# Optimization experiments

Hardware: AMD Instinct MI355X
Metric: run time of the kernel (lower is better)

Reference implementation:

```python
import jax, jax.numpy as jnp
import numpy as np

GN_EPS = 1e-5
LN_EPS = 1e-5
M_HEADS, N_LEVELS, N_POINTS, D_MODEL = 8, 3, 4, 256
HEAD_DIM = D_MODEL // M_HEADS


def conv1x1(x, w, b):
    return jnp.einsum('nchw,oc->nohw', x, w[:, :, 0, 0]) + b[None, :, None, None]


def conv3x3(x, w, b):
    y = jax.lax.conv_general_dilated(x, w, (1, 1), ((1, 1), (1, 1)),
                                     dimension_numbers=('NCHW', 'OIHW', 'NCHW'))
    return y + b[None, :, None, None]


def group_norm(x, w, b, groups=32):
    N, C, H, W = x.shape
    xg = x.reshape(N, groups, C // groups, H, W)
    mu = xg.mean((2, 3, 4), keepdims=True)
    var = xg.var((2, 3, 4), keepdims=True)
    xg = (xg - mu) / jnp.sqrt(var + GN_EPS)
    return xg.reshape(N, C, H, W) * w[None, :, None, None] + b[None, :, None, None]


def layer_norm(x, w, b):
    mu = x.mean(-1, keepdims=True)
    var = x.var(-1, keepdims=True)
    return (x - mu) / jnp.sqrt(var + LN_EPS) * w + b


def prelu(x, a):
    return jnp.where(x >= 0, x, a[0] * x)


def pos_sine(mask):
    # DETR PositionEmbeddingSine, num_pos_feats=128, normalize=True
    nm = (~mask).astype(jnp.float32)
    y_embed = jnp.cumsum(nm, 1)
    x_embed = jnp.cumsum(nm, 2)
    eps, scale = 1e-6, 2.0 * np.pi
    y_embed = y_embed / (y_embed[:, -1:, :] + eps) * scale
    x_embed = x_embed / (x_embed[:, :, -1:] + eps) * scale
    npf = D_MODEL // 2
    dim_t = 10000.0 ** (2.0 * (jnp.arange(npf) // 2).astype(jnp.float32) / npf)
    px = x_embed[..., None] / dim_t
    py = y_embed[..., None] / dim_t

    def il(p):
        return jnp.stack([jnp.sin(p[..., 0::2]), jnp.cos(p[..., 1::2])], -1).reshape(p.shape[0], p.shape[1], p.shape[2], -1)

    return jnp.transpose(jnp.concatenate([il(py), il(px)], -1), (0, 3, 1, 2))


def resize_mask_nearest(mask, h, w):
    H, W = mask.shape[1], mask.shape[2]
    iy = jnp.floor(jnp.arange(h) * (H / h)).astype(jnp.int32)
    ix = jnp.floor(jnp.arange(w) * (W / w)).astype(jnp.int32)
    return mask[:, iy][:, :, ix]


def bilinear_gather(v, x, y):
    # v: (N,M,D,H,W); x,y: (N,Lq,M,P) pixel coords; zero padding, align_corners=False
    N, M, D, H, W = v.shape
    Lq, P = x.shape[1], x.shape[3]
    x0f = jnp.floor(x)
    y0f = jnp.floor(y)
    wx = (x - x0f)[..., None]
    wy = (y - y0f)[..., None]
    x0i = x0f.astype(jnp.int32)
    y0i = y0f.astype(jnp.int32)
    flat = jnp.transpose(v, (0, 1, 3, 4, 2)).reshape(N, M, H * W, D)

    def gather(xi, yi):
        valid = (xi >= 0) & (xi < W) & (yi >= 0) & (yi < H)
        idx = jnp.clip(yi, 0, H - 1) * W + jnp.clip(xi, 0, W - 1)
        idx2 = jnp.transpose(idx, (0, 2, 1, 3)).reshape(N, M, Lq * P)
        g = jnp.take_along_axis(flat, idx2[..., None], axis=2)
        g = jnp.transpose(g.reshape(N, M, Lq, P, D), (0, 2, 1, 3, 4))
        return g * valid[..., None]

    g00 = gather(x0i, y0i)
    g01 = gather(x0i + 1, y0i)
    g10 = gather(x0i, y0i + 1)
    g11 = gather(x0i + 1, y0i + 1)
    return g00 * (1 - wx) * (1 - wy) + g01 * wx * (1 - wy) + g10 * (1 - wx) * wy + g11 * wx * wy


def _forward(x0, x1, x2, p3_w, p3_b, p4_w, p4_b, p5_w, p5_b,
             gn3_w, gn3_b, gn4_w, gn4_b, gn5_w, gn5_b, level_embed,
             so_w, so_b, aw_w, aw_b, vp_w, vp_b, op_w, op_b,
             ln1_w, ln1_b, ffn1_w, ffn1_b, ffn2_w, ffn2_b, ln2_w, ln2_b,
             d3_w, d3_b, d3_a, d4_w, d4_b, d4_a, d5_w, d5_b, d5_a,
             padding_masks):
    N = x0.shape[0]
    shapes = [(x0.shape[2], x0.shape[3]), (x1.shape[2], x1.shape[3]), (x2.shape[2], x2.shape[3])]
    p3 = group_norm(conv1x1(x0, p3_w, p3_b), gn3_w, gn3_b)
    p4 = group_norm(conv1x1(x1, p4_w, p4_b), gn4_w, gn4_b)
    p5 = group_norm(conv1x1(x2, p5_w, p5_b), gn5_w, gn5_b)
    srcs = [p3, p4, p5]
    masks = [resize_mask_nearest(padding_masks, H, W) for (H, W) in shapes]
    src_flat = jnp.concatenate([s.reshape(N, D_MODEL, -1).transpose(0, 2, 1) for s in srcs], 1)
    mask_flat = jnp.concatenate([m.reshape(N, -1) for m in masks], 1)
    pos_flat = jnp.concatenate(
        [pos_sine(m).reshape(N, D_MODEL, -1).transpose(0, 2, 1) + level_embed[l][None, None]
         for l, m in enumerate(masks)], 1)
    # valid ratios (N, 3, 2) as (w, h)
    vrs = []
    for (H, W), m in zip(shapes, masks):
        vh = jnp.sum((~m[:, :, 0]).astype(jnp.float32), 1) / H
        vw = jnp.sum((~m[:, 0, :]).astype(jnp.float32), 1) / W
        vrs.append(jnp.stack([vw, vh], -1))
    vr = jnp.stack(vrs, 1)
    # reference points (N, Lq, 3, 2)
    refs = []
    for lvl, (H, W) in enumerate(shapes):
        ry, rx = jnp.meshgrid(jnp.linspace(0.5, H - 0.5, H), jnp.linspace(0.5, W - 0.5, W), indexing='ij')
        ry = ry.reshape(-1)[None] / (vr[:, None, lvl, 1] * H)
        rx = rx.reshape(-1)[None] / (vr[:, None, lvl, 0] * W)
        refs.append(jnp.stack([rx, ry], -1))
    ref = jnp.concatenate(refs, 1)[:, :, None] * vr[:, None]

    # --- MSDeformAttn ---
    q = src_flat + pos_flat
    Lq = q.shape[1]
    value = src_flat @ vp_w.T + vp_b
    value = jnp.where(mask_flat[..., None], 0.0, value).reshape(N, Lq, M_HEADS, HEAD_DIM)
    off = (q @ so_w.T + so_b).reshape(N, Lq, M_HEADS, N_LEVELS, N_POINTS, 2)
    aw = jax.nn.softmax((q @ aw_w.T + aw_b).reshape(N, Lq, M_HEADS, N_LEVELS * N_POINTS), -1)
    aw = aw.reshape(N, Lq, M_HEADS, N_LEVELS, N_POINTS)
    norm = jnp.array([[W, H] for (H, W) in shapes], jnp.float32)
    loc = ref[:, :, None, :, None, :] + off / norm[None, None, None, :, None, :]
    out = jnp.zeros((N, Lq, M_HEADS, HEAD_DIM), value.dtype)
    start = 0
    for l, (H, W) in enumerate(shapes):
        vl = value[:, start:start + H * W].reshape(N, H, W, M_HEADS, HEAD_DIM)
        vl = jnp.transpose(vl, (0, 3, 4, 1, 2))  # (N, M, D, H, W)
        sx = loc[:, :, :, l, :, 0] * W - 0.5
        sy = loc[:, :, :, l, :, 1] * H - 0.5
        samp = bilinear_gather(vl, sx, sy)  # (N, Lq, M, P, D)
        out = out + jnp.einsum('nqmpd,nqmp->nqmd', samp, aw[:, :, :, l])
        start += H * W
    attn = out.reshape(N, Lq, D_MODEL) @ op_w.T + op_b

    src = layer_norm(src_flat + attn, ln1_w, ln1_b)
    ffn = jax.nn.relu(src @ ffn1_w.T + ffn1_b) @ ffn2_w.T + ffn2_b
    src = layer_norm(src + ffn, ln2_w, ln2_b)

    # take level-2 tokens back to spatial
    H2, W2 = shapes[2]
    start2 = shapes[0][0] * shapes[0][1] + shapes[1][0] * shapes[1][1]
    o = src[:, start2:start2 + H2 * W2].reshape(N, H2, W2, D_MODEL).transpose(0, 3, 1, 2)

    o = jax.image.resize(o, (N, D_MODEL) + shapes[0], 'bilinear', antialias=False) + prelu(conv3x3(x0, d3_w, d3_b), d3_a)
    o = jax.image.resize(o, (N, D_MODEL) + shapes[1], 'bilinear', antialias=False) + prelu(conv3x3(x1, d4_w, d4_b), d4_a)
    o = jax.image.resize(o, (N, D_MODEL) + shapes[2], 'bilinear', antialias=False) + prelu(conv3x3(x2, d5_w, d5_b), d5_a)
    return o


def setup_inputs():
    key = jax.random.key(0)
    ks = jax.random.split(key, 24)
    B, C = 2, 256

    def w(k, shape, sc=0.02):
        return jax.random.normal(k, shape, jnp.float32) * sc

    inp = {}
    inp['x0'] = jax.random.normal(ks[0], (B, 2048, 64, 64), jnp.float32)
    inp['x1'] = jax.random.normal(ks[1], (B, 2048, 32, 32), jnp.float32)
    inp['x2'] = jax.random.normal(ks[2], (B, 2048, 16, 16), jnp.float32)
    inp['padding_masks'] = jnp.zeros((B, 64, 64), bool)
    inp['p3_w'] = w(ks[3], (C, 2048, 1, 1)); inp['p3_b'] = jnp.zeros((C,))
    inp['p4_w'] = w(ks[4], (C, 2048, 1, 1)); inp['p4_b'] = jnp.zeros((C,))
    inp['p5_w'] = w(ks[5], (C, 2048, 1, 1)); inp['p5_b'] = jnp.zeros((C,))
    inp['gn3_w'] = jnp.ones((C,)); inp['gn3_b'] = jnp.zeros((C,))
    inp['gn4_w'] = jnp.ones((C,)); inp['gn4_b'] = jnp.zeros((C,))
    inp['gn5_w'] = jnp.ones((C,)); inp['gn5_b'] = jnp.zeros((C,))
    inp['level_embed'] = w(ks[6], (3, C), 1.0)
    inp['so_w'] = w(ks[7], (192, C)); inp['so_b'] = w(ks[8], (192,), 0.5)
    inp['aw_w'] = w(ks[9], (96, C)); inp['aw_b'] = jnp.zeros((96,))
    inp['vp_w'] = w(ks[10], (C, C)); inp['vp_b'] = jnp.zeros((C,))
    inp['op_w'] = w(ks[11], (C, C)); inp['op_b'] = jnp.zeros((C,))
    inp['ln1_w'] = jnp.ones((C,)); inp['ln1_b'] = jnp.zeros((C,))
    inp['ffn1_w'] = w(ks[12], (1024, C)); inp['ffn1_b'] = jnp.zeros((1024,))
    inp['ffn2_w'] = w(ks[13], (C, 1024)); inp['ffn2_b'] = jnp.zeros((C,))
    inp['ln2_w'] = jnp.ones((C,)); inp['ln2_b'] = jnp.zeros((C,))
    inp['d3_w'] = w(ks[14], (C, 2048, 3, 3)); inp['d3_b'] = jnp.zeros((C,)); inp['d3_a'] = jnp.full((1,), 0.25)
    inp['d4_w'] = w(ks[15], (C, 2048, 3, 3)); inp['d4_b'] = jnp.zeros((C,)); inp['d4_a'] = jnp.full((1,), 0.25)
    inp['d5_w'] = w(ks[16], (C, 2048, 3, 3)); inp['d5_b'] = jnp.zeros((C,)); inp['d5_a'] = jnp.full((1,), 0.25)
    return inp


def reference(x0, x1, x2, padding_masks, p3_w, p3_b, p4_w, p4_b, p5_w, p5_b,
              gn3_w, gn3_b, gn4_w, gn4_b, gn5_w, gn5_b, level_embed,
              so_w, so_b, aw_w, aw_b, vp_w, vp_b, op_w, op_b,
              ln1_w, ln1_b, ffn1_w, ffn1_b, ffn2_w, ffn2_b, ln2_w, ln2_b,
              d3_w, d3_b, d3_a, d4_w, d4_b, d4_a, d5_w, d5_b, d5_a):
    return _forward(x0, x1, x2, p3_w, p3_b, p4_w, p4_b, p5_w, p5_b,
                    gn3_w, gn3_b, gn4_w, gn4_b, gn5_w, gn5_b, level_embed,
                    so_w, so_b, aw_w, aw_b, vp_w, vp_b, op_w, op_b,
                    ln1_w, ln1_b, ffn1_w, ffn1_b, ffn2_w, ffn2_b, ln2_w, ln2_b,
                    d3_w, d3_b, d3_a, d4_w, d4_b, d4_a, d5_w, d5_b, d5_a,
                    padding_masks)
```

## Files before the change

### kernel.cpp

```cpp
#include <hip/hip_runtime.h>
#include <hip/hip_bf16.h>

#define NTOK 5376

typedef short bfrag __attribute__((ext_vector_type(8)));
typedef short bvec4 __attribute__((ext_vector_type(4)));
typedef float facc  __attribute__((ext_vector_type(4)));

__device__ __forceinline__ short f2bf(float f) {
  __hip_bfloat16 h = __float2bfloat16(f);
  return *reinterpret_cast<short*>(&h);
}
__device__ __forceinline__ float bf2f(short s) {
  union { unsigned int u; float f; } cv;
  cv.u = ((unsigned int)(unsigned short)s) << 16;
  return cv.f;
}

#define ASYNC_COPY16(gp, sp) \
  __builtin_amdgcn_global_load_lds((const __attribute__((address_space(1))) unsigned int*)(gp), \
                                   (__attribute__((address_space(3))) unsigned int*)(sp), 16, 0, 0)

__global__ __launch_bounds__(256) void init_all_kernel(
    const float* __restrict__ x0, const float* __restrict__ x1, const float* __restrict__ x2,
    short* __restrict__ xb0, short* __restrict__ xb1, short* __restrict__ xb2,
    const float* __restrict__ p3, const float* __restrict__ p4, const float* __restrict__ p5,
    const float* __restrict__ vp,
    const float* __restrict__ so, const float* __restrict__ aw, const float* __restrict__ op,
    const float* __restrict__ f1, const float* __restrict__ f2,
    const float* __restrict__ d3,
    short* __restrict__ pwb0, short* __restrict__ pwb1, short* __restrict__ pwb2,
    short* __restrict__ vpb,
    short* __restrict__ soT, short* __restrict__ awT, short* __restrict__ opT,
    short* __restrict__ f1T, short* __restrict__ f2T,
    short* __restrict__ w0)
{
  __shared__ float tile[64][65];
  __shared__ float tt[32][33];
  int b = blockIdx.x;
  if (b < 7168) {
    const float* x; short* xb; int H, Wshift;
    if (b < 4096)      { x = x0; xb = xb0; H = 64; Wshift = 6; }
    else if (b < 6144) { x = x1; xb = xb1; H = 32; Wshift = 5; b -= 4096; }
    else               { x = x2; xb = xb2; H = 16; Wshift = 4; b -= 6144; }
    int cin0 = (b & 31) << 6;
    int t1 = b >> 5;
    int y = t1 & (H - 1);
    int n = t1 >> Wshift;
    int W = 1 << Wshift;
    int elems = 64 << Wshift;
    for (int i = threadIdx.x; i < elems; i += 256) {
      int px = i & (W - 1), cl = i >> Wshift;
      tile[cl][px] = x[(((long)(n * 2048 + cin0 + cl)) * H + y) * W + px];
    }
    __syncthreads();
    int Hp = H + 2;
    for (int i = threadIdx.x; i < elems; i += 256) {
      int cl = i & 63, px = i >> 6;
      xb[(((long)(n * Hp + y + 1)) * Hp + (px + 1)) * 2048 + cin0 + cl] = f2bf(tile[cl][px]);
    }
    return;
  }
  b -= 7168;
  if (b < 6144) {
    const float* src; short* dst;
    if (b < 2048)      { src = p3; dst = pwb0; }
    else if (b < 4096) { src = p4; dst = pwb1; b -= 2048; }
    else               { src = p5; dst = pwb2; b -= 4096; }
    int idx = b * 256 + threadIdx.x;
    dst[idx] = f2bf(src[idx]);
    return;
  }
  b -= 6144;
  if (b < 256) {
    int idx = b * 256 + threadIdx.x;
    vpb[idx] = f2bf(vp[idx]);
    return;
  }
  b -= 256;
  if (b < 648) {
    const float* src; short* dst; int N, K, tb;
    if (b < 48)       { src = so; dst = soT; N = 192;  K = 256;  tb = b; }
    else if (b < 72)  { src = aw; dst = awT; N = 96;   K = 256;  tb = b - 48; }
    else if (b < 136) { src = op; dst = opT; N = 256;  K = 256;  tb = b - 72; }
    else if (b < 392) { src = f1; dst = f1T; N = 1024; K = 256;  tb = b - 136; }
    else              { src = f2; dst = f2T; N = 256;  K = 1024; tb = b - 392; }
    int ktiles = K >> 5;
    int tn = tb / ktiles, tk = tb % ktiles;
#pragma unroll
    for (int s = 0; s < 4; ++s) {
      int i = s * 256 + threadIdx.x;
      int r = i >> 5, c = i & 31;
      tt[r][c] = src[(long)(tn * 32 + r) * K + tk * 32 + c];
    }
    __syncthreads();
#pragma unroll
    for (int s = 0; s < 4; ++s) {
      int i = s * 256 + threadIdx.x;
      int r = i >> 5, c = i & 31;
      dst[(long)(tk * 32 + r) * N + tn * 32 + c] = f2bf(tt[c][r]);
    }
    return;
  }
  b -= 648;
  {
    int p = b * 256 + threadIdx.x;
    int oc = p >> 11, cin = p & 2047;
    float v[9];
#pragma unroll
    for (int t = 0; t < 9; ++t) v[t] = d3[(long)p * 9 + t];
#pragma unroll
    for (int ky = 0; ky < 3; ++ky)
#pragma unroll
      for (int kx = 0; kx < 3; ++kx)
        w0[((long)(ky * 256 + oc)) * 6144 + kx * 2048 + cin] = f2bf(v[ky * 3 + kx]);
  }
}

#define BUFSH 24576

__device__ __forceinline__ void conv3x3_pipe(short* lds,
    const short* __restrict__ xb, const short* __restrict__ wb,
    short* __restrict__ part, int Wshift, int HW2, int mt, int kb, int steps)
{
  int tid = threadIdx.x;
  int lane = tid & 63;
  int wid = tid >> 6;
  int wm = wid >> 2;
  int wn = wid & 3;
  int W = 1 << Wshift;
  int HW = 1 << (2 * Wshift);
  int px0 = mt * 128;
  int n = px0 >> (2 * Wshift);
  int rem = px0 & (HW - 1);
  int Hp = W + 2;
  long rowstride = (long)Hp * 2048;

  const short* agA[2];
  const short* bgB[4];
#pragma unroll
  for (int r = 0; r < 2; ++r) {
    int c = r * 512 + tid;
    int pl = c >> 3;
    int kc = (c & 7) ^ (pl & 7);
    int p = rem + pl;
    int yy = p >> Wshift, xx = p & (W - 1);
    agA[r] = xb + (((long)(n * Hp + yy)) * Hp + xx) * 2048 + kc * 8;
  }
#pragma unroll
  for (int r = 0; r < 4; ++r) {
    int c = r * 512 + tid;
    int pl = c >> 3;
    int kc = (c & 7) ^ (pl & 7);
    bgB[r] = wb + (long)pl * 6144 + kc * 8;
  }
  int ldst = (tid & 448) * 8;

  facc acc[4][4];
#pragma unroll
  for (int mi = 0; mi < 4; ++mi)
#pragma unroll
    for (int ni = 0; ni < 4; ++ni) acc[mi][ni] = (facc)(0.f);

  int arow[4], brow[4];
#pragma unroll
  for (int i = 0; i < 4; ++i) {
    arow[i] = (wm * 64 + i * 16 + (lane & 15)) * 64;
    brow[i] = 8192 + (wn * 64 + i * 16 + (lane & 15)) * 64;
  }

  auto ISSUE = [&](int it, short* db) {
    int ky = (it >= 192) ? 2 : ((it >= 96) ? 1 : 0);
    int kc96 = it - ky * 96;
    long aoff = (long)ky * rowstride + (long)kc96 * 64;
    long boff = (long)ky * 1572864 + (long)kc96 * 64;
    ASYNC_COPY16(agA[0] + aoff, db + ldst);
    ASYNC_COPY16(agA[1] + aoff, db + 4096 + ldst);
    ASYNC_COPY16(bgB[0] + boff, db + 8192 + ldst);
    ASYNC_COPY16(bgB[1] + boff, db + 12288 + ldst);
    ASYNC_COPY16(bgB[2] + boff, db + 16384 + ldst);
    ASYNC_COPY16(bgB[3] + boff, db + 20480 + ldst);
  };

  auto COMPUTE = [&](const short* buf) {
#pragma unroll
    for (int k0 = 0; k0 < 2; ++k0) {
      int slot8 = ((((k0 << 2) + (lane >> 4)) ^ (lane & 7)) << 3);
      bfrag af[4], bf4[4];
#pragma unroll
      for (int mi = 0; mi < 4; ++mi) af[mi] = *(const bfrag*)(buf + arow[mi] + slot8);
#pragma unroll
      for (int ni = 0; ni < 4; ++ni) bf4[ni] = *(const bfrag*)(buf + brow[ni] + slot8);
      __builtin_amdgcn_s_setprio(1);
#pragma unroll
      for (int mi = 0; mi < 4; ++mi)
#pragma unroll
        for (int ni = 0; ni < 4; ++ni)
          acc[mi][ni] = __builtin_amdgcn_mfma_f32_16x16x32_bf16(af[mi], bf4[ni], acc[mi][ni], 0, 0, 0);
      __builtin_amdgcn_s_setprio(0);
    }
  };

  short* b0 = lds;
  short* b1 = lds + BUFSH;
  short* b2 = lds + 2 * BUFSH;
  int it0 = kb * steps;

  ISSUE(it0, b0);
  ISSUE(it0 + 1, b1);
  asm volatile("s_waitcnt vmcnt(6)" ::: "memory");
  __builtin_amdgcn_s_barrier();

  for (int t = 0; t < steps - 2; ++t) {
    ISSUE(it0 + t + 2, b2);
    COMPUTE(b0);
    asm volatile("s_waitcnt vmcnt(6)" ::: "memory");
    __builtin_amdgcn_s_barrier();
    short* tmp = b0; b0 = b1; b1 = b2; b2 = tmp;
  }
  COMPUTE(b0);
  asm volatile("s_waitcnt vmcnt(0)" ::: "memory");
  __builtin_amdgcn_s_barrier();
  COMPUTE(b1);

  short* pp = part + ((long)kb * HW2 + px0) * 256;
#pragma unroll
  for (int mi = 0; mi < 4; ++mi) {
    int pl = wm * 64 + mi * 16 + ((lane >> 4) << 2);
#pragma unroll
    for (int ni = 0; ni < 4; ++ni) {
      int ol = wn * 64 + ni * 16 + (lane & 15);
#pragma unroll
      for (int r = 0; r < 4; ++r)
        pp[(long)(pl + r) * 256 + ol] = f2bf(acc[mi][ni][r]);
    }
  }
}

__global__ __launch_bounds__(512, 2) void conv0_kernel(
    const short* __restrict__ xb, const short* __restrict__ wb, short* __restrict__ part) {
  __shared__ __align__(16) short lds[3 * BUFSH];
  int b = blockIdx.x;
  conv3x3_pipe(lds, xb, wb, part, 6, 8192, b >> 2, b & 3, 72);
}

__global__ __launch_bounds__(512, 2) void conv12_kernel(
    const short* __restrict__ xb1, const short* __restrict__ w1, short* __restrict__ part1,
    const short* __restrict__ xb2, const short* __restrict__ w2, short* __restrict__ part2) {
  __shared__ __align__(16) short lds[3 * BUFSH];
  int b = blockIdx.x;
  if (b < 128) {
    conv3x3_pipe(lds, xb1, w1, part1, 5, 2048, b >> 3, b & 7, 36);
  } else {
    b -= 128;
    conv3x3_pipe(lds, xb2, w2, part2, 4, 512, b >> 3, b & 7, 36);
  }
}

__device__ __forceinline__ void reduce_body(int idx, const short* __restrict__ part,
    const float* __restrict__ bias, const float* __restrict__ alpha_p,
    short* __restrict__ out, int HW2, int hwshift, int KB) {
  int px = idx >> 8, oc = idx & 255;
  long step = (long)HW2 * 256;
  float s = 0.f;
  for (int kb = 0; kb < KB; ++kb) s += bf2f(part[kb * step + idx]);
  float v = s + bias[oc];
  float alpha = alpha_p[0];
  v = (v >= 0.f) ? v : alpha * v;
  int HW = 1 << hwshift;
  int n = px >> hwshift;
  int sp = px & (HW - 1);
  out[(((long)(n * 256 + oc)) << hwshift) + sp] = f2bf(v);
}

__device__ __forceinline__ void block_reduce2(float& s, float& s2) {
#pragma unroll
  for (int o = 32; o > 0; o >>= 1) {
    s  += __shfl_down(s, o, 64);
    s2 += __shfl_down(s2, o, 64);
  }
  __shared__ float r1[4], r2[4];
  int wid = threadIdx.x >> 6;
  int lane = threadIdx.x & 63;
  if (lane == 0) { r1[wid] = s; r2[wid] = s2; }
  __syncthreads();
  s  = r1[0] + r1[1] + r1[2] + r1[3];
  s2 = r2[0] + r2[1] + r2[2] + r2[3];
  __syncthreads();
}

__global__ __launch_bounds__(256) void reduce0_stats_w12_kernel(
    const short* __restrict__ part0, const float* __restrict__ d3_b,
    const float* __restrict__ d3_a, short* __restrict__ c0b,
    const short* __restrict__ srcb, float* __restrict__ stats,
    const float* __restrict__ d4, const float* __restrict__ d5,
    short* __restrict__ w1, short* __restrict__ w2) {
  int b = blockIdx.x;
  if (b < 8192) {
    reduce_body(b * 256 + threadIdx.x, part0, d3_b, d3_a, c0b, 8192, 12, 4);
    return;
  }
  b -= 8192;
  if (b < 192) {
    int n = b / 96, r = b % 96, l = r / 32, g = r % 32;
    int H, base;
    if (l == 0)      { H = 64; base = 0; }
    else if (l == 1) { H = 32; base = 4096; }
    else             { H = 16; base = 5120; }
    int HW = H * H;
    const short* p = srcb + ((long)n * NTOK + base) * 256 + g * 8;
    float s = 0.f, s2 = 0.f;
    for (int idx = threadIdx.x; idx < HW * 8; idx += 256) {
      int hw = idx >> 3, c = idx & 7;
      float v = bf2f(p[(long)hw * 256 + c]);
      s += v; s2 += v * v;
    }
    block_reduce2(s, s2);
    if (threadIdx.x == 0) {
      float cnt = (float)(HW * 8);
      float mu = s / cnt;
      float var = s2 / cnt - mu * mu;
      stats[b * 2]     = mu;
      stats[b * 2 + 1] = rsqrtf(var + 1e-5f);
    }
    return;
  }
  b -= 192;
  {
    const float* src; short* dst;
    if (b < 2048) { src = d4; dst = w1; } else { src = d5; dst = w2; b -= 2048; }
    int p = b * 256 + threadIdx.x;
    int oc = p >> 11, cin = p & 2047;
    float v[9];
#pragma unroll
    for (int t = 0; t < 9; ++t) v[t] = src[(long)p * 9 + t];
#pragma unroll
    for (int ky = 0; ky < 3; ++ky)
#pragma unroll
      for (int kx = 0; kx < 3; ++kx)
        dst[((long)(ky * 256 + oc)) * 6144 + kx * 2048 + cin] = f2bf(v[ky * 3 + kx]);
  }
}

__global__ __launch_bounds__(256) void reduce12_gn_kernel(
    const short* __restrict__ part1, const short* __restrict__ part2,
    const float* __restrict__ d4_b, const float* __restrict__ d4_a,
    const float* __restrict__ d5_b, const float* __restrict__ d5_a,
    short* __restrict__ c1b, short* __restrict__ c2b,
    short* __restrict__ srcb, const float* __restrict__ stats,
    const float* __restrict__ gw0, const float* __restrict__ gb0,
    const float* __restrict__ gw1, const float* __restrict__ gb1,
    const float* __restrict__ gw2, const float* __restrict__ gb2) {
  int b = blockIdx.x;
  if (b < 2048) { reduce_body(b * 256 + threadIdx.x, part1, d4_b, d4_a, c1b, 2048, 10, 8); return; }
  if (b < 2560) { reduce_body((b - 2048) * 256 + threadIdx.x, part2, d5_b, d5_a, c2b, 512, 8, 8); return; }
  b -= 2560;
  int idx = b * 256 + threadIdx.x;
  int row = idx >> 8, c = idx & 255;
  int n = row / NTOK, t = row % NTOK;
  int l; const float *gw, *gb;
  if (t < 4096)      { l = 0; gw = gw0; gb = gb0; }
  else if (t < 5120) { l = 1; gw = gw1; gb = gb1; }
  else               { l = 2; gw = gw2; gb = gb2; }
  int si = (n * 96 + l * 32 + (c >> 3)) * 2;
  float mu = stats[si], rstd = stats[si + 1];
  float v = (bf2f(srcb[idx]) - mu) * rstd * gw[c] + gb[c];
  srcb[idx] = f2bf(v);
}

__device__ __forceinline__ void conv1x1_body(short* As, short* Bs,
    const short* __restrict__ A, const short* __restrict__ Bw,
    const float* __restrict__ bias, short* __restrict__ Cb,
    int Wshift, int Hp, int shift2, int tokbase, int ocb, int py)
{
  int tid = threadIdx.x;
  int lane = tid & 63;
  int wid = tid >> 6;
  int wm = wid >> 1, wn = wid & 1;
  int px0 = py * 128;

  const short* ag0[4];
  const short* bg0[4];
#pragma unroll
  for (int j = 0; j < 4; ++j) {
    int c = j * 256 + tid;
    int pl = c >> 3;
    int kc = (c & 7) ^ (pl & 7);
    int p = px0 + pl;
    int n = p >> shift2;
    int remp = p & ((1 << shift2) - 1);
    int W = 1 << Wshift;
    int yy = remp >> Wshift, xx = remp & (W - 1);
    long arow = (((long)(n * Hp + yy + 1)) * Hp + (xx + 1)) * 2048;
    ag0[j] = A + arow + kc * 8;
    bg0[j] = Bw + (long)(ocb * 128 + pl) * 2048 + kc * 8;
  }

  facc acc[4][4];
#pragma unroll
  for (int mi = 0; mi < 4; ++mi)
#pragma unroll
    for (int ni = 0; ni < 4; ++ni) acc[mi][ni] = (facc)(0.f);

  for (int it = 0; it < 32; ++it) {
    long off = (long)it * 64;
#pragma unroll
    for (int j = 0; j < 4; ++j) {
      ASYNC_COPY16(ag0[j] + off, As + (j * 256 + (tid & 192)) * 8);
// ... 248 lines not shown
  }
  float s1r = x, s2r = x * x;
  block_reduce2(s1r, s2r);
  float mu = s1r * (1.f / 256.f);
  float rstd = rsqrtf(s2r * (1.f / 256.f) - mu * mu + 1e-5f);
  x = (x - mu) * rstd * ln1_w[tid] + ln1_b[tid];
  x1s[tid] = x;
  __syncthreads();

  {
    int j0 = tid * 4;
    float a0 = 0.f, a1 = 0.f, a2 = 0.f, a3 = 0.f;
#pragma unroll 4
    for (int k = 0; k < 256; ++k) {
      bvec4 wv = *(const bvec4*)(f1T + (long)k * 1024 + j0);
      float xv = x1s[k];
      a0 += xv * bf2f(wv[0]); a1 += xv * bf2f(wv[1]);
      a2 += xv * bf2f(wv[2]); a3 += xv * bf2f(wv[3]);
    }
    hids[j0 + 0] = fmaxf(a0 + ffn1_b[j0 + 0], 0.f);
    hids[j0 + 1] = fmaxf(a1 + ffn1_b[j0 + 1], 0.f);
    hids[j0 + 2] = fmaxf(a2 + ffn1_b[j0 + 2], 0.f);
    hids[j0 + 3] = fmaxf(a3 + ffn1_b[j0 + 3], 0.f);
  }
  __syncthreads();

  float y;
  {
    float s0 = 0.f, s1 = 0.f, s2 = 0.f, s3 = 0.f;
#pragma unroll 4
    for (int k = 0; k < 1024; k += 4) {
      s0 += hids[k]     * bf2f(f2T[(long)k * 256 + tid]);
      s1 += hids[k + 1] * bf2f(f2T[(long)(k + 1) * 256 + tid]);
      s2 += hids[k + 2] * bf2f(f2T[(long)(k + 2) * 256 + tid]);
      s3 += hids[k + 3] * bf2f(f2T[(long)(k + 3) * 256 + tid]);
    }
    y = x + (s0 + s1) + (s2 + s3) + ffn2_b[tid];
  }
  s1r = y; s2r = y * y;
  block_reduce2(s1r, s2r);
  mu = s1r * (1.f / 256.f);
  rstd = rsqrtf(s2r * (1.f / 256.f) - mu * mu + 1e-5f);
  src2c[(long)b * 256 + tid] = (y - mu) * rstd * ln2_w[tid] + ln2_b[tid];
}

__global__ __launch_bounds__(256) void fused_resize_kernel(
    const float* __restrict__ src2c, const short* __restrict__ c0b,
    const short* __restrict__ c1b, const short* __restrict__ c2b,
    float* __restrict__ out) {
  int idx = blockIdx.x * 256 + threadIdx.x;
  int x = idx & 15, y = (idx >> 4) & 15, c = (idx >> 8) & 255, n = idx >> 16;
  const float* sbase = src2c + (long)n * 65536 + c;
  const short* c0p = c0b + ((long)(n * 256 + c) << 12);
  const short* c1p = c1b + ((long)(n * 256 + c) << 10);
  float s64 = 0.f;
#pragma unroll
  for (int dy = 0; dy < 4; ++dy) {
    int Y = 4 * y + dy;
    float sy = fminf(fmaxf(0.25f * Y - 0.375f, 0.f), 15.f);
    int y0 = (int)sy;
    int y1 = min(y0 + 1, 15);
    float wy = sy - y0;
#pragma unroll
    for (int dx = 0; dx < 4; ++dx) {
      int X = 4 * x + dx;
      float sx = fminf(fmaxf(0.25f * X - 0.375f, 0.f), 15.f);
      int x0 = (int)sx;
      int x1 = min(x0 + 1, 15);
      float wx = sx - x0;
      float v = (sbase[(y0 * 16 + x0) * 256] * (1.f - wx) + sbase[(y0 * 16 + x1) * 256] * wx) * (1.f - wy) +
                (sbase[(y1 * 16 + x0) * 256] * (1.f - wx) + sbase[(y1 * 16 + x1) * 256] * wx) * wy;
      s64 += v + bf2f(c0p[Y * 64 + X]);
    }
  }
  float s32 = bf2f(c1p[(2 * y) * 32 + 2 * x]) + bf2f(c1p[(2 * y) * 32 + 2 * x + 1]) +
              bf2f(c1p[(2 * y + 1) * 32 + 2 * x]) + bf2f(c1p[(2 * y + 1) * 32 + 2 * x + 1]);
  out[idx] = 0.0625f * s64 + 0.25f * s32 + bf2f(c2b[idx]);
}

extern "C" void kernel_launch(void* const* d_in, const int* in_sizes, int n_in,
                              void* d_out, int out_size, void* d_ws, size_t ws_size,
                              hipStream_t stream) {
  (void)in_sizes; (void)n_in; (void)out_size; (void)ws_size;
  const float* x0   = (const float*)d_in[0];
  const float* x1   = (const float*)d_in[1];
  const float* x2   = (const float*)d_in[2];
  const float* p3_w = (const float*)d_in[4];
  const float* p3_b = (const float*)d_in[5];
  const float* p4_w = (const float*)d_in[6];
  const float* p4_b = (const float*)d_in[7];
  const float* p5_w = (const float*)d_in[8];
  const float* p5_b = (const float*)d_in[9];
  const float* gn3_w = (const float*)d_in[10];
  const float* gn3_b = (const float*)d_in[11];
  const float* gn4_w = (const float*)d_in[12];
  const float* gn4_b = (const float*)d_in[13];
  const float* gn5_w = (const float*)d_in[14];
  const float* gn5_b = (const float*)d_in[15];
  const float* level_embed = (const float*)d_in[16];
  const float* so_w = (const float*)d_in[17];
  const float* so_b = (const float*)d_in[18];
  const float* aw_w = (const float*)d_in[19];
  const float* aw_b = (const float*)d_in[20];
  const float* vp_w = (const float*)d_in[21];
  const float* vp_b = (const float*)d_in[22];
  const float* op_w = (const float*)d_in[23];
  const float* op_b = (const float*)d_in[24];
  const float* ln1_w = (const float*)d_in[25];
  const float* ln1_b = (const float*)d_in[26];
  const float* ffn1_w = (const float*)d_in[27];
  const float* ffn1_b = (const float*)d_in[28];
  const float* ffn2_w = (const float*)d_in[29];
  const float* ffn2_b = (const float*)d_in[30];
  const float* ln2_w = (const float*)d_in[31];
  const float* ln2_b = (const float*)d_in[32];
  const float* d3_w = (const float*)d_in[33];
  const float* d3_b = (const float*)d_in[34];
  const float* d3_a = (const float*)d_in[35];
  const float* d4_w = (const float*)d_in[36];
  const float* d4_b = (const float*)d_in[37];
  const float* d4_a = (const float*)d_in[38];
  const float* d5_w = (const float*)d_in[39];
  const float* d5_b = (const float*)d_in[40];
  const float* d5_a = (const float*)d_in[41];

  float* ws = (float*)d_ws;
  short* xb0   = (short*)(ws + 0L);
  short* xb1   = (short*)(ws + 8921088L);
  short* xb2   = (short*)(ws + 11288576L);
  short* part0 = (short*)(ws + 11952128L);
  short* pwb0  = (short*)(ws + 14442496L);
  short* pwb1  = (short*)(ws + 14704640L);
  short* pwb2  = (short*)(ws + 14966784L);
  short* wbuf  = (short*)(ws + 16146432L);
  short* c0b   = (short*)(ws + 17457152L);
  short* w1    = (short*)(ws + 0L);
  short* w2    = (short*)(ws + 2359296L);
  short* part1 = (short*)(ws + 4718592L);
  short* part2 = (short*)(ws + 6815744L);
  short* srcb  = (short*)(ws + 18505728L);
  short* c1b   = (short*)(ws + 19881984L);
  short* c2b   = (short*)(ws + 20144128L);
  short* vpb   = (short*)(ws + 20209664L);
  short* soT   = (short*)(ws + 20242432L);
  short* awT   = (short*)(ws + 20267008L);
  short* opT   = (short*)(ws + 20279296L);
  short* f1T   = (short*)(ws + 20312064L);
  short* f2T   = (short*)(ws + 20443136L);
  float* stats = ws + 20574208L;
  float* val   = ws + 0L;
  float* src2c = ws + 2752512L;

  dim3 blk(256);
  dim3 blk2(512);

  hipMemsetAsync(xb0, 0, (size_t)11952128 * 4, stream);
  init_all_kernel<<<16264, blk, 0, stream>>>(x0, x1, x2, xb0, xb1, xb2,
      p3_w, p4_w, p5_w, vp_w, so_w, aw_w, op_w, ffn1_w, ffn2_w, d3_w,
      pwb0, pwb1, pwb2, vpb, soT, awT, opT, f1T, f2T, wbuf);
  conv1x1_all_kernel<<<168, blk, 0, stream>>>(xb0, xb1, xb2, pwb0, pwb1, pwb2,
      p3_b, p4_b, p5_b, srcb);
  conv0_kernel<<<256, blk2, 0, stream>>>(xb0, wbuf, part0);
  reduce0_stats_w12_kernel<<<12480, blk, 0, stream>>>(part0, d3_b, d3_a, c0b,
      srcb, stats, d4_w, d5_w, w1, w2);
  conv12_kernel<<<160, blk2, 0, stream>>>(xb1, w1, part1, xb2, w2, part2);
  reduce12_gn_kernel<<<13312, blk, 0, stream>>>(part1, part2, d4_b, d4_a,
      d5_b, d5_a, c1b, c2b, srcb, stats,
      gn3_w, gn3_b, gn4_w, gn4_b, gn5_w, gn5_b);
  valproj_kernel<<<dim3(2, 84), blk, 0, stream>>>(srcb, vpb, vp_b, val);
  tail_kernel<<<512, blk, 0, stream>>>(srcb, val, level_embed,
      soT, so_b, awT, aw_b, opT, op_b, ln1_w, ln1_b,
      f1T, ffn1_b, f2T, ffn2_b, ln2_w, ln2_b, src2c);
  fused_resize_kernel<<<512, blk, 0, stream>>>(src2c, c0b, c1b, c2b, (float*)d_out);
}
```

Measured before the change: 549.9 us.

## Retile conv3x3 GEMM to 256x128 tiles with 4-wave blocks and register double-buffering

The implicit-GEMM 3x3 convolution now uses 256 threads (4 waves) per block. Each block covers a 256-pixel by 128-output-channel tile with a K-step of 32 instead of 64. Each wave holds an 8x4 grid of MFMA accumulators. LDS fragment loads for the next step are issued before the MFMAs of the current step (register double-buffering), with a 4-deep LDS ring and a new rotated swizzle. The goal is higher MFMA work per LDS load and better overlap of LDS reads with compute, at the cost of more registers, one block per CU, and twice as many pipeline steps and barriers.

After: 566.6 us. 3.0% more time.

```diff
diff --git a/kernel.cpp b/kernel.cpp
--- a/kernel.cpp
+++ b/kernel.cpp
@@ -117,116 +117,139 @@
   }
 }
 
-#define BUFSH 24576
-
-__device__ __forceinline__ void conv3x3_pipe(short* lds,
+#define BUF2 12288
+
+__device__ __forceinline__ void conv3x3_pipe2(short* lds,
     const short* __restrict__ xb, const short* __restrict__ wb,
-    short* __restrict__ part, int Wshift, int HW2, int mt, int kb, int steps)
+    short* __restrict__ part, int Wshift, int HW2, int mt, int ocb, int kb, int steps)
 {
   int tid = threadIdx.x;
   int lane = tid & 63;
   int wid = tid >> 6;
-  int wm = wid >> 2;
-  int wn = wid & 3;
+  int wm = wid >> 1, wn = wid & 1;
   int W = 1 << Wshift;
   int HW = 1 << (2 * Wshift);
-  int px0 = mt * 128;
+  int px0 = mt * 256;
   int n = px0 >> (2 * Wshift);
   int rem = px0 & (HW - 1);
   int Hp = W + 2;
   long rowstride = (long)Hp * 2048;
 
-  const short* agA[2];
-  const short* bgB[4];
-#pragma unroll
-  for (int r = 0; r < 2; ++r) {
-    int c = r * 512 + tid;
-    int pl = c >> 3;
-    int kc = (c & 7) ^ (pl & 7);
-    int p = rem + pl;
+  const short* ag[4];
+  const short* bg[2];
+#pragma unroll
+  for (int j = 0; j < 4; ++j) {
+    int c = j * 256 + tid;
+    int r = c >> 2, s = c & 3;
+    int gsrc = (s - (r >> 1)) & 3;
+    int p = rem + r;
     int yy = p >> Wshift, xx = p & (W - 1);
-    agA[r] = xb + (((long)(n * Hp + yy)) * Hp + xx) * 2048 + kc * 8;
-  }
-#pragma unroll
-  for (int r = 0; r < 4; ++r) {
-    int c = r * 512 + tid;
-    int pl = c >> 3;
-    int kc = (c & 7) ^ (pl & 7);
-    bgB[r] = wb + (long)pl * 6144 + kc * 8;
-  }
-  int ldst = (tid & 448) * 8;
-
-  facc acc[4][4];
-#pragma unroll
-  for (int mi = 0; mi < 4; ++mi)
+    ag[j] = xb + (((long)(n * Hp + yy)) * Hp + xx) * 2048 + gsrc * 8;
+  }
+#pragma unroll
+  for (int j = 0; j < 2; ++j) {
+    int c = j * 256 + tid;
+    int r = c >> 2, s = c & 3;
+    int gsrc = (s - (r >> 1)) & 3;
+    bg[j] = wb + (long)(ocb * 128 + r) * 6144 + gsrc * 8;
+  }
+  int lbase = (tid & 192) * 8;
+
+  int aoff[8], boff[4];
+#pragma unroll
+  for (int mi = 0; mi < 8; ++mi) {
+    int r = wm * 128 + mi * 16 + (lane & 15);
+    int slot = ((lane >> 4) + (r >> 1)) & 3;
+    aoff[mi] = r * 32 + slot * 8;
+  }
+#pragma unroll
+  for (int ni = 0; ni < 4; ++ni) {
+    int r = wn * 64 + ni * 16 + (lane & 15);
+    int slot = ((lane >> 4) + (r >> 1)) & 3;
+    boff[ni] = 8192 + r * 32 + slot * 8;
+  }
+
+  facc acc[8][4];
+#pragma unroll
+  for (int mi = 0; mi < 8; ++mi)
 #pragma unroll
     for (int ni = 0; ni < 4; ++ni) acc[mi][ni] = (facc)(0.f);
 
-  int arow[4], brow[4];
-#pragma unroll
-  for (int i = 0; i < 4; ++i) {
-    arow[i] = (wm * 64 + i * 16 + (lane & 15)) * 64;
-    brow[i] = 8192 + (wn * 64 + i * 16 + (lane & 15)) * 64;
-  }
-
-  auto ISSUE = [&](int it, short* db) {
-    int ky = (it >= 192) ? 2 : ((it >= 96) ? 1 : 0);
-    int kc96 = it - ky * 96;
-    long aoff = (long)ky * rowstride + (long)kc96 * 64;
-    long boff = (long)ky * 1572864 + (long)kc96 * 64;
-    ASYNC_COPY16(agA[0] + aoff, db + ldst);
-    ASYNC_COPY16(agA[1] + aoff, db + 4096 + ldst);
-    ASYNC_COPY16(bgB[0] + boff, db + 8192 + ldst);
-    ASYNC_COPY16(bgB[1] + boff, db + 12288 + ldst);
-    ASYNC_COPY16(bgB[2] + boff, db + 16384 + ldst);
-    ASYNC_COPY16(bgB[3] + boff, db + 20480 + ldst);
+  auto ISSUE = [&](int it, int bufi) {
+    short* db = lds + bufi * BUF2;
+    int ky = (it >= 384) ? 2 : ((it >= 192) ? 1 : 0);
+    int kc = it - ky * 192;
+    long ao = (long)ky * rowstride + (long)kc * 32;
+    long bo = (long)ky * 1572864 + (long)kc * 32;
+    ASYNC_COPY16(ag[0] + ao, db + lbase);
+    ASYNC_COPY16(ag[1] + ao, db + 2048 + lbase);
+    ASYNC_COPY16(ag[2] + ao, db + 4096 + lbase);
+    ASYNC_COPY16(ag[3] + ao, db + 6144 + lbase);
+    ASYNC_COPY16(bg[0] + bo, db + 8192 + lbase);
+    ASYNC_COPY16(bg[1] + bo, db + 10240 + lbase);
   };
 
-  auto COMPUTE = [&](const short* buf) {
-#pragma unroll
-    for (int k0 = 0; k0 < 2; ++k0) {
-      int slot8 = ((((k0 << 2) + (lane >> 4)) ^ (lane & 7)) << 3);
-      bfrag af[4], bf4[4];
-#pragma unroll
-      for (int mi = 0; mi < 4; ++mi) af[mi] = *(const bfrag*)(buf + arow[mi] + slot8);
-#pragma unroll
-      for (int ni = 0; ni < 4; ++ni) bf4[ni] = *(const bfrag*)(buf + brow[ni] + slot8);
-      __builtin_amdgcn_s_setprio(1);
-#pragma unroll
-      for (int mi = 0; mi < 4; ++mi)
-#pragma unroll
-        for (int ni = 0; ni < 4; ++ni)
-          acc[mi][ni] = __builtin_amdgcn_mfma_f32_16x16x32_bf16(af[mi], bf4[ni], acc[mi][ni], 0, 0, 0);
-      __builtin_amdgcn_s_setprio(0);
-    }
+  auto LOADF = [&](int bufi, bfrag* af, bfrag* bf) {
+    const short* buf = lds + bufi * BUF2;
+#pragma unroll
+    for (int mi = 0; mi < 8; ++mi) af[mi] = *(const bfrag*)(buf + aoff[mi]);
+#pragma unroll
+    for (int ni = 0; ni < 4; ++ni) bf[ni] = *(const bfrag*)(buf + boff[ni]);
   };
 
-  short* b0 = lds;
-  short* b1 = lds + BUFSH;
-  short* b2 = lds + 2 * BUFSH;
+  auto DOMFMA = [&](bfrag* af, bfrag* bf) {
+    __builtin_amdgcn_s_setprio(1);
+#pragma unroll
+    for (int mi = 0; mi < 8; ++mi)
+#pragma unroll
+      for (int ni = 0; ni < 4; ++ni)
+        acc[mi][ni] = __builtin_amdgcn_mfma_f32_16x16x32_bf16(af[mi], bf[ni], acc[mi][ni], 0, 0, 0);
+    __builtin_amdgcn_s_setprio(0);
+  };
+
   int it0 = kb * steps;
-
-  ISSUE(it0, b0);
-  ISSUE(it0 + 1, b1);
+  bfrag afE[8], bfE[4], afO[8], bfO[4];
+
+  ISSUE(it0 + 0, 0);
+  ISSUE(it0 + 1, 1);
   asm volatile("s_waitcnt vmcnt(6)" ::: "memory");
   __builtin_amdgcn_s_barrier();
-
-  for (int t = 0; t < steps - 2; ++t) {
-    ISSUE(it0 + t + 2, b2);
-    COMPUTE(b0);
+  LOADF(0, afE, bfE);
+  ISSUE(it0 + 2, 2);
+  asm volatile("s_waitcnt vmcnt(6)" ::: "memory");
+  __builtin_amdgcn_s_barrier();
+
+  int t = 0;
+  for (; t + 5 < steps; t += 2) {
+    ISSUE(it0 + t + 3, (t + 3) & 3);
+    LOADF((t + 1) & 3, afO, bfO);
+    DOMFMA(afE, bfE);
     asm volatile("s_waitcnt vmcnt(6)" ::: "memory");
     __builtin_amdgcn_s_barrier();
-    short* tmp = b0; b0 = b1; b1 = b2; b2 = tmp;
-  }
-  COMPUTE(b0);
+
+    ISSUE(it0 + t + 4, (t + 4) & 3);
+    LOADF((t + 2) & 3, afE, bfE);
+    DOMFMA(afO, bfO);
+    asm volatile("s_waitcnt vmcnt(6)" ::: "memory");
+    __builtin_amdgcn_s_barrier();
+  }
+  ISSUE(it0 + steps - 1, (steps - 1) & 3);
+  LOADF((steps - 3) & 3, afO, bfO);
+  DOMFMA(afE, bfE);
+  asm volatile("s_waitcnt vmcnt(6)" ::: "memory");
+  __builtin_amdgcn_s_barrier();
+  LOADF((steps - 2) & 3, afE, bfE);
+  DOMFMA(afO, bfO);
   asm volatile("s_waitcnt vmcnt(0)" ::: "memory");
   __builtin_amdgcn_s_barrier();
-  COMPUTE(b1);
-
-  short* pp = part + ((long)kb * HW2 + px0) * 256;
-#pragma unroll
-  for (int mi = 0; mi < 4; ++mi) {
-    int pl = wm * 64 + mi * 16 + ((lane >> 4) << 2);
+  LOADF((steps - 1) & 3, afO, bfO);
+  DOMFMA(afE, bfE);
+  DOMFMA(afO, bfO);
+
+  short* pp = part + ((long)kb * HW2 + px0) * 256 + ocb * 128;
+#pragma unroll
+  for (int mi = 0; mi < 8; ++mi) {
+    int pl = wm * 128 + mi * 16 + ((lane >> 4) << 2);
 #pragma unroll
     for (int ni = 0; ni < 4; ++ni) {
       int ol = wn * 64 + ni * 16 + (lane & 15);
@@ -237,23 +260,23 @@
   }
 }
 
-__global__ __launch_bounds__(512, 2) void conv0_kernel(
+__global__ __launch_bounds__(256, 1) void conv0_kernel(
     const short* __restrict__ xb, const short* __restrict__ wb, short* __restrict__ part) {
-  __shared__ __align__(16) short lds[3 * BUFSH];
+  __shared__ __align__(16) short lds[4 * BUF2];
   int b = blockIdx.x;
-  conv3x3_pipe(lds, xb, wb, part, 6, 8192, b >> 2, b & 3, 72);
-}
-
-__global__ __launch_bounds__(512, 2) void conv12_kernel(
+  conv3x3_pipe2(lds, xb, wb, part, 6, 8192, (b >> 2) & 31, b >> 7, b & 3, 144);
+}
+
+__global__ __launch_bounds__(256, 1) void conv12_kernel(
     const short* __restrict__ xb1, const short* __restrict__ w1, short* __restrict__ part1,
     const short* __restrict__ xb2, const short* __restrict__ w2, short* __restrict__ part2) {
-  __shared__ __align__(16) short lds[3 * BUFSH];
+  __shared__ __align__(16) short lds[4 * BUF2];
   int b = blockIdx.x;
   if (b < 128) {
-    conv3x3_pipe(lds, xb1, w1, part1, 5, 2048, b >> 3, b & 7, 36);
+    conv3x3_pipe2(lds, xb1, w1, part1, 5, 2048, (b >> 3) & 7, b >> 6, b & 7, 72);
   } else {
     b -= 128;
-    conv3x3_pipe(lds, xb2, w2, part2, 4, 512, b >> 3, b & 7, 36);
+    conv3x3_pipe2(lds, xb2, w2, part2, 4, 512, (b >> 3) & 1, b >> 4, b & 7, 72);
   }
 }
 
@@ -808,7 +831,6 @@
   float* src2c = ws + 2752512L;
 
   dim3 blk(256);
-  dim3 blk2(512);
 
   hipMemsetAsync(xb0, 0, (size_t)11952128 * 4, stream);
   init_all_kernel<<<16264, blk, 0, stream>>>(x0, x1, x2, xb0, xb1, xb2,
@@ -816,10 +838,10 @@
       pwb0, pwb1, pwb2, vpb, soT, awT, opT, f1T, f2T, wbuf);
   conv1x1_all_kernel<<<168, blk, 0, stream>>>(xb0, xb1, xb2, pwb0, pwb1, pwb2,
       p3_b, p4_b, p5_b, srcb);
-  conv0_kernel<<<256, blk2, 0, stream>>>(xb0, wbuf, part0);
+  conv0_kernel<<<256, blk, 0, stream>>>(xb0, wbuf, part0);
   reduce0_stats_w12_kernel<<<12480, blk, 0, stream>>>(part0, d3_b, d3_a, c0b,
       srcb, stats, d4_w, d5_w, w1, w2);
-  conv12_kernel<<<160, blk2, 0, stream>>>(xb1, w1, part1, xb2, w2, part2);
+  conv12_kernel<<<160, blk, 0, stream>>>(xb1, w1, part1, xb2, w2, part2);
   reduce12_gn_kernel<<<13312, blk, 0, stream>>>(part1, part2, d4_b, d4_a,
       d5_b, d5_a, c1b, c2b, srcb, stats,
       gn3_w, gn3_b, gn4_w, gn4_b, gn5_w, gn5_b);
```

## Interleave async loads with MFMA halves in 3x3 conv pipeline

Applied to the files above, without the earlier changes.

Restructures the conv3x3 main loop so each K-step splits into two N-halves. The A tile and the two B-halves' global-to-LDS copies are issued between fragment reads and MFMA groups, with finer vmcnt waits and two barriers per step. The B fragment mapping changes so each wave's columns interleave across 64-column groups. The aim is to hide load issue latency behind compute and smooth LDS/VMEM traffic. The cost is an extra barrier per iteration and more register pressure from holding two A fragment sets.

New measurement: 537.4 us. -2.3%, faster.

```diff
diff --git a/kernel.cpp b/kernel.cpp
--- a/kernel.cpp
+++ b/kernel.cpp
@@ -117,11 +117,11 @@
   }
 }
 
-#define BUFSH 24576
-
-__device__ __forceinline__ void conv3x3_pipe(short* lds,
+#define BUF3 24576
+
+__device__ __forceinline__ void conv3x3_pipe3(short* lds,
     const short* __restrict__ xb, const short* __restrict__ wb,
-    short* __restrict__ part, int Wshift, int HW2, int mt, int kb, int steps)
+    short* __restrict__ part, int Wshift, int HW2, int mt, int kb, int T)
 {
   int tid = threadIdx.x;
   int lane = tid & 63;
@@ -136,8 +136,7 @@
   int Hp = W + 2;
   long rowstride = (long)Hp * 2048;
 
-  const short* agA[2];
-  const short* bgB[4];
+  const short* ag[2];
 #pragma unroll
   for (int r = 0; r < 2; ++r) {
     int c = r * 512 + tid;
@@ -145,115 +144,160 @@
     int kc = (c & 7) ^ (pl & 7);
     int p = rem + pl;
     int yy = p >> Wshift, xx = p & (W - 1);
-    agA[r] = xb + (((long)(n * Hp + yy)) * Hp + xx) * 2048 + kc * 8;
-  }
+    ag[r] = xb + (((long)(n * Hp + yy)) * Hp + xx) * 2048 + kc * 8;
+  }
+  const short* bg[4];
 #pragma unroll
   for (int r = 0; r < 4; ++r) {
     int c = r * 512 + tid;
     int pl = c >> 3;
     int kc = (c & 7) ^ (pl & 7);
-    bgB[r] = wb + (long)pl * 6144 + kc * 8;
+    bg[r] = wb + (long)pl * 6144 + kc * 8;
   }
   int ldst = (tid & 448) * 8;
-
-  facc acc[4][4];
-#pragma unroll
-  for (int mi = 0; mi < 4; ++mi)
-#pragma unroll
-    for (int ni = 0; ni < 4; ++ni) acc[mi][ni] = (facc)(0.f);
 
   int arow[4], brow[4];
 #pragma unroll
   for (int i = 0; i < 4; ++i) {
     arow[i] = (wm * 64 + i * 16 + (lane & 15)) * 64;
-    brow[i] = 8192 + (wn * 64 + i * 16 + (lane & 15)) * 64;
-  }
-
-  auto ISSUE = [&](int it, short* db) {
+    brow[i] = 8192 + (i * 64 + wn * 16 + (lane & 15)) * 64;
+  }
+  int kcs[2];
+#pragma unroll
+  for (int k0 = 0; k0 < 2; ++k0)
+    kcs[k0] = ((((k0 << 2) + (lane >> 4)) ^ (lane & 7)) << 3);
+
+  facc acc[4][4];
+#pragma unroll
+  for (int mi = 0; mi < 4; ++mi)
+#pragma unroll
+    for (int ni = 0; ni < 4; ++ni) acc[mi][ni] = (facc)(0.f);
+
+  auto KYOFF = [&](int it, long& ao, long& bo) {
     int ky = (it >= 192) ? 2 : ((it >= 96) ? 1 : 0);
     int kc96 = it - ky * 96;
-    long aoff = (long)ky * rowstride + (long)kc96 * 64;
-    long boff = (long)ky * 1572864 + (long)kc96 * 64;
-    ASYNC_COPY16(agA[0] + aoff, db + ldst);
-    ASYNC_COPY16(agA[1] + aoff, db + 4096 + ldst);
-    ASYNC_COPY16(bgB[0] + boff, db + 8192 + ldst);
-    ASYNC_COPY16(bgB[1] + boff, db + 12288 + ldst);
-    ASYNC_COPY16(bgB[2] + boff, db + 16384 + ldst);
-    ASYNC_COPY16(bgB[3] + boff, db + 20480 + ldst);
+    ao = (long)ky * rowstride + (long)kc96 * 64;
+    bo = (long)ky * 1572864 + (long)kc96 * 64;
   };
-
-  auto COMPUTE = [&](const short* buf) {
-#pragma unroll
-    for (int k0 = 0; k0 < 2; ++k0) {
-      int slot8 = ((((k0 << 2) + (lane >> 4)) ^ (lane & 7)) << 3);
-      bfrag af[4], bf4[4];
-#pragma unroll
-      for (int mi = 0; mi < 4; ++mi) af[mi] = *(const bfrag*)(buf + arow[mi] + slot8);
-#pragma unroll
-      for (int ni = 0; ni < 4; ++ni) bf4[ni] = *(const bfrag*)(buf + brow[ni] + slot8);
-      __builtin_amdgcn_s_setprio(1);
-#pragma unroll
-      for (int mi = 0; mi < 4; ++mi)
-#pragma unroll
-        for (int ni = 0; ni < 4; ++ni)
-          acc[mi][ni] = __builtin_amdgcn_mfma_f32_16x16x32_bf16(af[mi], bf4[ni], acc[mi][ni], 0, 0, 0);
-      __builtin_amdgcn_s_setprio(0);
-    }
+  auto ISSUE_A = [&](int it, int bufi) {
+    long ao, bo; KYOFF(it, ao, bo); (void)bo;
+    short* db = lds + bufi * BUF3;
+    ASYNC_COPY16(ag[0] + ao, db + ldst);
+    ASYNC_COPY16(ag[1] + ao, db + 4096 + ldst);
   };
-
-  short* b0 = lds;
-  short* b1 = lds + BUFSH;
-  short* b2 = lds + 2 * BUFSH;
-  int it0 = kb * steps;
-
-  ISSUE(it0, b0);
-  ISSUE(it0 + 1, b1);
-  asm volatile("s_waitcnt vmcnt(6)" ::: "memory");
+  auto ISSUE_B0 = [&](int it, int bufi) {
+    long ao, bo; KYOFF(it, ao, bo); (void)ao;
+    short* db = lds + bufi * BUF3;
+    ASYNC_COPY16(bg[0] + bo, db + 8192 + ldst);
+    ASYNC_COPY16(bg[1] + bo, db + 12288 + ldst);
+  };
+  auto ISSUE_B1 = [&](int it, int bufi) {
+    long ao, bo; KYOFF(it, ao, bo); (void)ao;
+    short* db = lds + bufi * BUF3;
+    ASYNC_COPY16(bg[2] + bo, db + 16384 + ldst);
+    ASYNC_COPY16(bg[3] + bo, db + 20480 + ldst);
+  };
+
+  auto RD_A = [&](int bufi, int k0, bfrag* af) {
+    const short* buf = lds + bufi * BUF3;
+#pragma unroll
+    for (int mi = 0; mi < 4; ++mi) af[mi] = *(const bfrag*)(buf + arow[mi] + kcs[k0]);
+  };
+  auto RD_B = [&](int bufi, int k0, int nh, bfrag* bf) {
+    const short* buf = lds + bufi * BUF3;
+#pragma unroll
+    for (int j = 0; j < 2; ++j) bf[j] = *(const bfrag*)(buf + brow[2 * nh + j] + kcs[k0]);
+  };
+  auto MM = [&](bfrag* af, bfrag* bf, int nh) {
+    __builtin_amdgcn_s_setprio(1);
+#pragma unroll
+    for (int mi = 0; mi < 4; ++mi)
+#pragma unroll
+      for (int j = 0; j < 2; ++j)
+        acc[mi][2 * nh + j] = __builtin_amdgcn_mfma_f32_16x16x32_bf16(af[mi], bf[j], acc[mi][2 * nh + j], 0, 0, 0);
+    __builtin_amdgcn_s_setprio(0);
+  };
+
+  int it0 = kb * T;
+  bfrag a0[4], a1[4], b0[2], b1[2];
+
+  ISSUE_A(it0 + 0, 0); ISSUE_B0(it0 + 0, 0); ISSUE_B1(it0 + 0, 0);
+  ISSUE_A(it0 + 1, 1); ISSUE_B0(it0 + 1, 1); ISSUE_B1(it0 + 1, 1);
+  asm volatile("s_waitcnt vmcnt(8)" ::: "memory");
   __builtin_amdgcn_s_barrier();
 
-  for (int t = 0; t < steps - 2; ++t) {
-    ISSUE(it0 + t + 2, b2);
-    COMPUTE(b0);
+  int cur = 0;
+  for (int t = 0; t < T - 2; ++t) {
+    int nxt = cur + 2; if (nxt >= 3) nxt -= 3;
+    int itn = it0 + t + 2;
+    RD_A(cur, 0, a0); RD_B(cur, 0, 0, b0);
+    ISSUE_A(itn, nxt);
+    MM(a0, b0, 0);
+    RD_A(cur, 1, a1); RD_B(cur, 1, 0, b1);
+    ISSUE_B0(itn, nxt);
+    MM(a1, b1, 0);
+    asm volatile("s_waitcnt vmcnt(10)" ::: "memory");
+    __builtin_amdgcn_s_barrier();
+    RD_B(cur, 0, 1, b0);
+    ISSUE_B1(itn, nxt);
+    MM(a0, b0, 1);
+    RD_B(cur, 1, 1, b1);
+    MM(a1, b1, 1);
+    asm volatile("s_waitcnt vmcnt(8)" ::: "memory");
+    __builtin_amdgcn_s_barrier();
+    if (++cur == 3) cur = 0;
+  }
+  {
+    RD_A(cur, 0, a0); RD_B(cur, 0, 0, b0); MM(a0, b0, 0);
+    RD_A(cur, 1, a1); RD_B(cur, 1, 0, b1); MM(a1, b1, 0);
     asm volatile("s_waitcnt vmcnt(6)" ::: "memory");
     __builtin_amdgcn_s_barrier();
-    short* tmp = b0; b0 = b1; b1 = b2; b2 = tmp;
-  }
-  COMPUTE(b0);
-  asm volatile("s_waitcnt vmcnt(0)" ::: "memory");
-  __builtin_amdgcn_s_barrier();
-  COMPUTE(b1);
+    RD_B(cur, 0, 1, b0); MM(a0, b0, 1);
+    RD_B(cur, 1, 1, b1); MM(a1, b1, 1);
+    asm volatile("s_waitcnt vmcnt(2)" ::: "memory");
+    __builtin_amdgcn_s_barrier();
+    if (++cur == 3) cur = 0;
+  }
+  {
+    RD_A(cur, 0, a0); RD_B(cur, 0, 0, b0); MM(a0, b0, 0);
+    RD_A(cur, 1, a1); RD_B(cur, 1, 0, b1); MM(a1, b1, 0);
+    asm volatile("s_waitcnt vmcnt(0)" ::: "memory");
+    __builtin_amdgcn_s_barrier();
+    RD_B(cur, 0, 1, b0); MM(a0, b0, 1);
+    RD_B(cur, 1, 1, b1); MM(a1, b1, 1);
+  }
 
   short* pp = part + ((long)kb * HW2 + px0) * 256;
 #pragma unroll
   for (int mi = 0; mi < 4; ++mi) {
     int pl = wm * 64 + mi * 16 + ((lane >> 4) << 2);
 #pragma unroll
-    for (int ni = 0; ni < 4; ++ni) {
-      int ol = wn * 64 + ni * 16 + (lane & 15);
+    for (int nj = 0; nj < 4; ++nj) {
+      int ol = nj * 64 + wn * 16 + (lane & 15);
 #pragma unroll
       for (int r = 0; r < 4; ++r)
-        pp[(long)(pl + r) * 256 + ol] = f2bf(acc[mi][ni][r]);
+        pp[(long)(pl + r) * 256 + ol] = f2bf(acc[mi][nj][r]);
     }
   }
 }
 
 __global__ __launch_bounds__(512, 2) void conv0_kernel(
     const short* __restrict__ xb, const short* __restrict__ wb, short* __restrict__ part) {
-  __shared__ __align__(16) short lds[3 * BUFSH];
+  __shared__ __align__(16) short lds[3 * BUF3];
   int b = blockIdx.x;
-  conv3x3_pipe(lds, xb, wb, part, 6, 8192, b >> 2, b & 3, 72);
+  conv3x3_pipe3(lds, xb, wb, part, 6, 8192, b >> 2, b & 3, 72);
 }
 
 __global__ __launch_bounds__(512, 2) void conv12_kernel(
     const short* __restrict__ xb1, const short* __restrict__ w1, short* __restrict__ part1,
     const short* __restrict__ xb2, const short* __restrict__ w2, short* __restrict__ part2) {
-  __shared__ __align__(16) short lds[3 * BUFSH];
+  __shared__ __align__(16) short lds[3 * BUF3];
   int b = blockIdx.x;
   if (b < 128) {
-    conv3x3_pipe(lds, xb1, w1, part1, 5, 2048, b >> 3, b & 7, 36);
+    conv3x3_pipe3(lds, xb1, w1, part1, 5, 2048, b >> 3, b & 7, 36);
   } else {
     b -= 128;
-    conv3x3_pipe(lds, xb2, w2, part2, 4, 512, b >> 3, b & 7, 36);
+    conv3x3_pipe3(lds, xb2, w2, part2, 4, 512, b >> 3, b & 7, 36);
   }
 }
 
```
